# Kernel optimization log

Hardware: AMD Instinct MI355X
Metric: run time of the kernel (lower is better)

The kernel has to match this reference:

```python
import jax, jax.numpy as jnp
import numpy as np

NUM_MASKS = 255   # loop ids 0..254; id 255 is background
NUM_SEG = 256     # segment table size per batch element (ids 0..255)


def setup_inputs() -> dict:
    key = jax.random.key(0)
    k1, k2 = jax.random.split(key)
    b, c, h, w = 8, 256, 128, 128
    x = jax.random.normal(k1, (b, c, h, w), dtype=jnp.float32)
    mask = jax.random.randint(k2, (b, 1, h, w), 0, 256).astype(jnp.float32)
    return {"x": x, "mask": mask}


def reference(x, mask):
    b, c, h, w = x.shape
    hw = h * w
    # nearest interpolation to (h, w) is identity (mask already at that size)
    ids = mask.reshape(b, hw).astype(jnp.int32)          # (b, hw) segment ids 0..255
    x_sig = jax.nn.sigmoid(x.reshape(b, c, hw))          # (b, c, hw)

    # single-pass segment reduce: per-(batch, id) sums and pixel counts
    seg = (ids + jnp.arange(b, dtype=jnp.int32)[:, None] * NUM_SEG).reshape(-1)  # (b*hw,)
    counts = jax.ops.segment_sum(jnp.ones((b * hw,), x_sig.dtype), seg,
                                 num_segments=b * NUM_SEG).reshape(b, NUM_SEG)   # (b, 256)
    vals = x_sig.transpose(0, 2, 1).reshape(b * hw, c)                            # (b*hw, c)
    sums = jax.ops.segment_sum(vals, seg, num_segments=b * NUM_SEG)
    sums = sums.reshape(b, NUM_SEG, c)                                            # (b, 256, c)
    avg = sums / jnp.maximum(counts, 1.0)[:, :, None]                             # (b, 256, c)

    # gather per-pixel segment average; id 255 keeps label 0 (loop only covers 0..254)
    label = jnp.take_along_axis(avg, ids[:, :, None], axis=1)                     # (b, hw, c)
    is_bg = (ids == NUM_MASKS)[:, :, None]                                        # (b, hw, 1)
    label = jnp.where(is_bg, 0.0, label).transpose(0, 2, 1)                       # (b, c, hw)

    # ignore_bg=True: zero sigmoid activations on background pixels
    x_sig = jnp.where(is_bg.transpose(0, 2, 1), 0.0, x_sig)

    return jnp.mean((x_sig - label) ** 2)
```

## Files before the change

### kernel.cpp

```cpp
#include <hip/hip_runtime.h>

#define B 8
#define C 256
#define HW 16384
#define NSEG 256
#define NBLK (B * C)
#define NCH 32
#define CHUNK (HW / NCH)


typedef unsigned short ushort8 __attribute__((ext_vector_type(8)));

__device__ __forceinline__ float sigmoidf(float x) {
    return 1.0f / (1.0f + __expf(-x));
}

__global__ __launch_bounds__(256) void hist_kernel(const float* __restrict__ mask,
                                                   int* __restrict__ hist,
                                                   unsigned char* __restrict__ ids8) {
    __shared__ int h[NSEG];
    const int blk = blockIdx.x;
    const int b = blk >> 5, ch = blk & 31;
    const int t = threadIdx.x;
    h[t] = 0;
    __syncthreads();

    const float2* m2 = (const float2*)(mask + (size_t)b * HW + ch * CHUNK);
    uchar2* o2 = (uchar2*)(ids8 + (size_t)b * HW + ch * CHUNK);
    float2 v = m2[t];
    int i0 = (int)v.x, i1 = (int)v.y;
    o2[t] = make_uchar2((unsigned char)i0, (unsigned char)i1);
    atomicAdd(&h[i0], 1);
    atomicAdd(&h[i1], 1);
    __syncthreads();
    hist[blk * NSEG + t] = h[t];
}

__global__ __launch_bounds__(256) void assign_kernel(const unsigned char* __restrict__ ids8,
                                                     const int* __restrict__ hist,
                                                     int* __restrict__ starts_g,
                                                     unsigned short* __restrict__ permt) {
    __shared__ int sc[NSEG];
    __shared__ int cnt[NSEG];
    __shared__ int off[NSEG];
    const int blk = blockIdx.x;
    const int b = blk >> 5, ch = blk & 31;
    const int t = threadIdx.x;

    int tot = 0, pre = 0;
    for (int c2 = 0; c2 < NCH; ++c2) {
        int v = hist[((b << 5) + c2) * NSEG + t];
        tot += v;
        if (c2 < ch) pre += v;
    }
    cnt[t] = tot;
    sc[t] = tot;
    __syncthreads();
    for (int o = 1; o < NSEG; o <<= 1) {
        int v = (t >= o) ? sc[t - o] : 0;
        __syncthreads();
        sc[t] += v;
        __syncthreads();
    }
    int st = sc[t] - cnt[t];
    off[t] = st + pre;
    if (ch == 0) starts_g[b * NSEG + t] = st;
    __syncthreads();

    const unsigned char* idc = ids8 + (size_t)b * HW + ch * CHUNK;
    for (int j = 0; j < CHUNK / 256; ++j) {
        int pi = j * 256 + t;
        int id = idc[pi];
        int pos = atomicAdd(&off[id], 1);
        int p = ch * CHUNK + pi;
        int sidx = (pos & ~4095) | (((pos >> 3) & 7) << 9) | (((pos >> 6) & 63) << 3) | (pos & 7);
        permt[(size_t)b * HW + sidx] = (unsigned short)p;
    }
}

__global__ __launch_bounds__(256) void main_kernel(const float* __restrict__ x,
                                                   const unsigned short* __restrict__ permt,
                                                   const int* __restrict__ starts_g,
                                                   double* __restrict__ partials) {
    __shared__ float xs[HW];
    __shared__ int st[NSEG + 1];
    __shared__ float bS[NSEG];
    __shared__ float bQ[NSEG];
    __shared__ double wsum[4];

    const int bid = blockIdx.x;
    const int b = bid >> 8;
    const int t = threadIdx.x;

    const float* xrow = x + (size_t)bid * HW;
    for (int j = 0; j < 16; ++j) {
        int o = j * 1024 + t * 4;
        __builtin_amdgcn_global_load_lds(
            (const __attribute__((address_space(1))) void*)(xrow + o),
            (__attribute__((address_space(3))) void*)(xs + o), 16, 0, 0);
    }

    bS[t] = 0.0f;
    bQ[t] = 0.0f;
    st[t] = starts_g[b * NSEG + t];
    if (t == 0) st[NSEG] = HW;
    __syncthreads();

    int pos = t * 64;
    int lo = 0, hi = NSEG + 1;
    while (hi - lo > 1) {
        int mid = (lo + hi) >> 1;
        if (st[mid] <= pos) lo = mid; else hi = mid;
    }
    int s = lo;
    int nxt = st[s + 1];

    const ushort8* pr = (const ushort8*)(permt + (size_t)b * HW);
    const int w = t >> 6, l = t & 63;
    float S = 0.0f, Q = 0.0f;
    for (int j4 = 0; j4 < 8; ++j4) {
        ushort8 pp = pr[(w << 9) + (j4 << 6) + l];
        #pragma unroll
        for (int k = 0; k < 8; ++k) {
            int p = pp[k];
            float e = sigmoidf(xs[p]);
            if (pos >= nxt) {
                atomicAdd(&bS[s], S);
                atomicAdd(&bQ[s], Q);
                S = 0.0f; Q = 0.0f;
                do { ++s; } while (st[s + 1] <= pos);
                nxt = st[s + 1];
            }
            S += e;
            Q += e * e;
            ++pos;
        }
    }
    atomicAdd(&bS[s], S);
    atomicAdd(&bQ[s], Q);
    __syncthreads();

    double p = 0.0;
    if (t < NSEG - 1) {
        int n = st[t + 1] - st[t];
        if (n > 0) {
            double Sd = (double)bS[t], Qd = (double)bQ[t];
            p = Qd - Sd * Sd / (double)n;
        }
    }
    #pragma unroll
    for (int o = 32; o > 0; o >>= 1) p += __shfl_down(p, o);
    const int lane = t & 63, wv = t >> 6;
    if (lane == 0) wsum[wv] = p;
    __syncthreads();
    if (t == 0) partials[bid] = wsum[0] + wsum[1] + wsum[2] + wsum[3];
}

__global__ __launch_bounds__(256) void final_kernel(const double* __restrict__ partials,
                                                    float* __restrict__ out) {
    __shared__ double wsum[4];
    const int t = threadIdx.x;
    double p = 0.0;
    #pragma unroll
    for (int j = 0; j < NBLK / 256; ++j) p += partials[j * 256 + t];
    #pragma unroll
    for (int o = 32; o > 0; o >>= 1) p += __shfl_down(p, o);
    const int lane = t & 63, w = t >> 6;
    if (lane == 0) wsum[w] = p;
    __syncthreads();
    if (t == 0) {
        double total = wsum[0] + wsum[1] + wsum[2] + wsum[3];
        out[0] = (float)(total / (double)((size_t)B * C * HW));
    }
}

extern "C" void kernel_launch(void* const* d_in, const int* in_sizes, int n_in,
                              void* d_out, int out_size, void* d_ws, size_t ws_size,
                              hipStream_t stream) {
    const float* x = (const float*)d_in[0];
    const float* mask = (const float*)d_in[1];
    float* out = (float*)d_out;

    char* ws = (char*)d_ws;
    int* hist = (int*)ws;
    unsigned char* ids8 = (unsigned char*)(ws + 262144);
    int* starts = (int*)(ws + 393216);
    unsigned short* permt = (unsigned short*)(ws + 401408);
    double* partials = (double*)(ws + 663552);

    hist_kernel<<<B * NCH, 256, 0, stream>>>(mask, hist, ids8);
    assign_kernel<<<B * NCH, 256, 0, stream>>>(ids8, hist, starts, permt);
    main_kernel<<<NBLK, 256, 0, stream>>>(x, permt, starts, partials);
    final_kernel<<<1, 256, 0, stream>>>(partials, out);
}
```

Before: 228.2 us.

## Split each row into halves with global per-segment atomics to raise occupancy

Each (batch, channel) row is now handled by two blocks that each stage only half the pixels in LDS. This halves LDS use per block and allows more resident blocks per CU. Per-segment sums and squares are accumulated with global float atomics into zeroed buffers, and a new two-stage final reduction combines them using the full-row segment counts. It also switches the sigmoid to a hardware reciprocal and preloads the permutation vectors before the barrier. In exchange it adds global atomic traffic, an extra kernel launch, and nondeterministic float summation order.

```diff
diff --git a/kernel.cpp b/kernel.cpp
--- a/kernel.cpp
+++ b/kernel.cpp
@@ -3,21 +3,26 @@
 #define B 8
 #define C 256
 #define HW 16384
+#define HALF 8192
 #define NSEG 256
-#define NBLK (B * C)
 #define NCH 32
-#define CHUNK (HW / NCH)
+#define CHUNK 512
+#define NROW (B * C)
+#define NMAIN (NROW * 2)
 
 
 typedef unsigned short ushort8 __attribute__((ext_vector_type(8)));
 
 __device__ __forceinline__ float sigmoidf(float x) {
-    return 1.0f / (1.0f + __expf(-x));
+    float e = __expf(-x);
+    return __builtin_amdgcn_rcpf(1.0f + e);
 }
 
 __global__ __launch_bounds__(256) void hist_kernel(const float* __restrict__ mask,
                                                    int* __restrict__ hist,
-                                                   unsigned char* __restrict__ ids8) {
+                                                   unsigned char* __restrict__ ids8,
+                                                   float* __restrict__ Sg,
+                                                   float* __restrict__ Qg) {
     __shared__ int h[NSEG];
     const int blk = blockIdx.x;
     const int b = blk >> 5, ch = blk & 31;
@@ -32,29 +37,39 @@
     o2[t] = make_uchar2((unsigned char)i0, (unsigned char)i1);
     atomicAdd(&h[i0], 1);
     atomicAdd(&h[i1], 1);
+
+    float4 z = {0.0f, 0.0f, 0.0f, 0.0f};
+    float4* s4 = (float4*)(Sg + (size_t)blk * 2048);
+    float4* q4 = (float4*)(Qg + (size_t)blk * 2048);
+    #pragma unroll
+    for (int j = 0; j < 2; ++j) { s4[j * 256 + t] = z; q4[j * 256 + t] = z; }
+
     __syncthreads();
     hist[blk * NSEG + t] = h[t];
 }
 
 __global__ __launch_bounds__(256) void assign_kernel(const unsigned char* __restrict__ ids8,
                                                      const int* __restrict__ hist,
-                                                     int* __restrict__ starts_g,
+                                                     int* __restrict__ starts_h,
+                                                     int* __restrict__ counts_g,
                                                      unsigned short* __restrict__ permt) {
     __shared__ int sc[NSEG];
-    __shared__ int cnt[NSEG];
     __shared__ int off[NSEG];
     const int blk = blockIdx.x;
     const int b = blk >> 5, ch = blk & 31;
-    const int t = threadIdx.x;
-
-    int tot = 0, pre = 0;
+    const int half = ch >> 4;
+    const int t = threadIdx.x;
+
+    int tot = 0, tot_h = 0, pre = 0;
     for (int c2 = 0; c2 < NCH; ++c2) {
         int v = hist[((b << 5) + c2) * NSEG + t];
         tot += v;
-        if (c2 < ch) pre += v;
-    }
-    cnt[t] = tot;
-    sc[t] = tot;
+        if ((c2 >> 4) == half) {
+            tot_h += v;
+            if (c2 < ch) pre += v;
+        }
+    }
+    sc[t] = tot_h;
     __syncthreads();
     for (int o = 1; o < NSEG; o <<= 1) {
         int v = (t >= o) ? sc[t - o] : 0;
@@ -62,51 +77,57 @@
         sc[t] += v;
         __syncthreads();
     }
-    int st = sc[t] - cnt[t];
+    int st = sc[t] - tot_h;
     off[t] = st + pre;
-    if (ch == 0) starts_g[b * NSEG + t] = st;
+    if ((ch & 15) == 0) starts_h[(b * 2 + half) * NSEG + t] = st;
+    if (ch == 0) counts_g[b * NSEG + t] = tot;
     __syncthreads();
 
     const unsigned char* idc = ids8 + (size_t)b * HW + ch * CHUNK;
-    for (int j = 0; j < CHUNK / 256; ++j) {
+    for (int j = 0; j < 2; ++j) {
         int pi = j * 256 + t;
         int id = idc[pi];
         int pos = atomicAdd(&off[id], 1);
-        int p = ch * CHUNK + pi;
-        int sidx = (pos & ~4095) | (((pos >> 3) & 7) << 9) | (((pos >> 6) & 63) << 3) | (pos & 7);
-        permt[(size_t)b * HW + sidx] = (unsigned short)p;
-    }
-}
-
-__global__ __launch_bounds__(256) void main_kernel(const float* __restrict__ x,
-                                                   const unsigned short* __restrict__ permt,
-                                                   const int* __restrict__ starts_g,
-                                                   double* __restrict__ partials) {
-    __shared__ float xs[HW];
-    __shared__ int st[NSEG + 1];
-    __shared__ float bS[NSEG];
-    __shared__ float bQ[NSEG];
-    __shared__ double wsum[4];
+        int p = (ch * CHUNK + pi) & (HALF - 1);
+        int sidx = ((pos >> 11) << 11) | (((pos >> 3) & 3) << 9) | (((pos >> 5) & 63) << 3) | (pos & 7);
+        permt[(size_t)(b * 2 + half) * HALF + sidx] = (unsigned short)p;
+    }
+}
+
+__global__ __launch_bounds__(256, 4) void main_kernel(const float* __restrict__ x,
+                                                      const unsigned short* __restrict__ permt,
+                                                      const int* __restrict__ starts_h,
+                                                      float* __restrict__ Sg,
+                                                      float* __restrict__ Qg) {
+    __shared__ float xs[HALF];
+    __shared__ int st[NSEG + 2];
 
     const int bid = blockIdx.x;
-    const int b = bid >> 8;
-    const int t = threadIdx.x;
-
-    const float* xrow = x + (size_t)bid * HW;
-    for (int j = 0; j < 16; ++j) {
+    const int rowpair = bid >> 1;
+    const int half = bid & 1;
+    const int b = rowpair >> 8;
+    const int t = threadIdx.x;
+    const int w = t >> 6, l = t & 63;
+
+    const float* xsrc = x + (size_t)rowpair * HW + half * HALF;
+    for (int j = 0; j < 8; ++j) {
         int o = j * 1024 + t * 4;
         __builtin_amdgcn_global_load_lds(
-            (const __attribute__((address_space(1))) void*)(xrow + o),
+            (const __attribute__((address_space(1))) void*)(xsrc + o),
             (__attribute__((address_space(3))) void*)(xs + o), 16, 0, 0);
     }
 
-    bS[t] = 0.0f;
-    bQ[t] = 0.0f;
-    st[t] = starts_g[b * NSEG + t];
-    if (t == 0) st[NSEG] = HW;
-    __syncthreads();
-
-    int pos = t * 64;
+    const ushort8* pr = (const ushort8*)(permt + (size_t)(b * 2 + half) * HALF);
+    ushort8 pp0 = pr[(w << 8) + (0 << 6) + l];
+    ushort8 pp1 = pr[(w << 8) + (1 << 6) + l];
+    ushort8 pp2 = pr[(w << 8) + (2 << 6) + l];
+    ushort8 pp3 = pr[(w << 8) + (3 << 6) + l];
+
+    st[t] = starts_h[(b * 2 + half) * NSEG + t];
+    if (t == 0) st[NSEG] = HALF;
+    __syncthreads();
+
+    int pos = t * 32;
     int lo = 0, hi = NSEG + 1;
     while (hi - lo > 1) {
         int mid = (lo + hi) >> 1;
@@ -115,63 +136,61 @@
     int s = lo;
     int nxt = st[s + 1];
 
-    const ushort8* pr = (const ushort8*)(permt + (size_t)b * HW);
-    const int w = t >> 6, l = t & 63;
+    float* SgRow = Sg + (size_t)rowpair * NSEG;
+    float* QgRow = Qg + (size_t)rowpair * NSEG;
     float S = 0.0f, Q = 0.0f;
-    for (int j4 = 0; j4 < 8; ++j4) {
-        ushort8 pp = pr[(w << 9) + (j4 << 6) + l];
-        #pragma unroll
-        for (int k = 0; k < 8; ++k) {
-            int p = pp[k];
-            float e = sigmoidf(xs[p]);
-            if (pos >= nxt) {
-                atomicAdd(&bS[s], S);
-                atomicAdd(&bQ[s], Q);
-                S = 0.0f; Q = 0.0f;
-                do { ++s; } while (st[s + 1] <= pos);
-                nxt = st[s + 1];
-            }
-            S += e;
-            Q += e * e;
-            ++pos;
+
+    #define DO8(PP)                                              \
+        _Pragma("unroll")                                        \
+        for (int k = 0; k < 8; ++k) {                            \
+            if (pos == nxt) {                                    \
+                atomicAdd(&SgRow[s], S);                         \
+                atomicAdd(&QgRow[s], Q);                         \
+                S = 0.0f; Q = 0.0f;                              \
+                do { ++s; } while (st[s + 1] <= pos);            \
+                nxt = st[s + 1];                                 \
+            }                                                    \
+            float e = sigmoidf(xs[PP[k]]);                       \
+            S += e; Q += e * e; ++pos;                           \
         }
-    }
-    atomicAdd(&bS[s], S);
-    atomicAdd(&bQ[s], Q);
-    __syncthreads();
-
-    double p = 0.0;
-    if (t < NSEG - 1) {
-        int n = st[t + 1] - st[t];
-        if (n > 0) {
-            double Sd = (double)bS[t], Qd = (double)bQ[t];
-            p = Qd - Sd * Sd / (double)n;
+    DO8(pp0) DO8(pp1) DO8(pp2) DO8(pp3)
+    #undef DO8
+
+    atomicAdd(&SgRow[s], S);
+    atomicAdd(&QgRow[s], Q);
+}
+
+__global__ __launch_bounds__(256) void final1_kernel(const float* __restrict__ Sg,
+                                                     const float* __restrict__ Qg,
+                                                     const int* __restrict__ counts_g,
+                                                     double* __restrict__ partials) {
+    __shared__ double wsum[4];
+    const int blk = blockIdx.x, t = threadIdx.x;
+    double acc = 0.0;
+    for (int j = 0; j < 32; ++j) {
+        int bin = blk * 8192 + j * 256 + t;
+        int row = bin >> 8, s = bin & 255, b = row >> 8;
+        int n = counts_g[b * NSEG + s];
+        if (s < NSEG - 1 && n > 0) {
+            double S = (double)Sg[bin], Q = (double)Qg[bin];
+            acc += Q - S * S / (double)n;
         }
     }
+    #pragma unroll
+    for (int o = 32; o > 0; o >>= 1) acc += __shfl_down(acc, o);
+    const int lane = t & 63, w = t >> 6;
+    if (lane == 0) wsum[w] = acc;
+    __syncthreads();
+    if (t == 0) partials[blk] = wsum[0] + wsum[1] + wsum[2] + wsum[3];
+}
+
+__global__ __launch_bounds__(64) void final2_kernel(const double* __restrict__ partials,
+                                                    float* __restrict__ out) {
+    const int t = threadIdx.x;
+    double p = partials[t];
     #pragma unroll
     for (int o = 32; o > 0; o >>= 1) p += __shfl_down(p, o);
-    const int lane = t & 63, wv = t >> 6;
-    if (lane == 0) wsum[wv] = p;
-    __syncthreads();
-    if (t == 0) partials[bid] = wsum[0] + wsum[1] + wsum[2] + wsum[3];
-}
-
-__global__ __launch_bounds__(256) void final_kernel(const double* __restrict__ partials,
-                                                    float* __restrict__ out) {
-    __shared__ double wsum[4];
-    const int t = threadIdx.x;
-    double p = 0.0;
-    #pragma unroll
-    for (int j = 0; j < NBLK / 256; ++j) p += partials[j * 256 + t];
-    #pragma unroll
-    for (int o = 32; o > 0; o >>= 1) p += __shfl_down(p, o);
-    const int lane = t & 63, w = t >> 6;
-    if (lane == 0) wsum[w] = p;
-    __syncthreads();
-    if (t == 0) {
-        double total = wsum[0] + wsum[1] + wsum[2] + wsum[3];
-        out[0] = (float)(total / (double)((size_t)B * C * HW));
-    }
+    if (t == 0) out[0] = (float)(p / (double)((size_t)B * C * HW));
 }
 
 extern "C" void kernel_launch(void* const* d_in, const int* in_sizes, int n_in,
@@ -184,12 +203,16 @@
     char* ws = (char*)d_ws;
     int* hist = (int*)ws;
     unsigned char* ids8 = (unsigned char*)(ws + 262144);
-    int* starts = (int*)(ws + 393216);
-    unsigned short* permt = (unsigned short*)(ws + 401408);
-    double* partials = (double*)(ws + 663552);
-
-    hist_kernel<<<B * NCH, 256, 0, stream>>>(mask, hist, ids8);
-    assign_kernel<<<B * NCH, 256, 0, stream>>>(ids8, hist, starts, permt);
-    main_kernel<<<NBLK, 256, 0, stream>>>(x, permt, starts, partials);
-    final_kernel<<<1, 256, 0, stream>>>(partials, out);
-}
+    int* starts_h = (int*)(ws + 393216);
+    int* counts_g = (int*)(ws + 409600);
+    unsigned short* permt = (unsigned short*)(ws + 417792);
+    float* Sg = (float*)(ws + 679936);
+    float* Qg = (float*)(ws + 2777088);
+    double* partials = (double*)(ws + 4874240);
+
+    hist_kernel<<<B * NCH, 256, 0, stream>>>(mask, hist, ids8, Sg, Qg);
+    assign_kernel<<<B * NCH, 256, 0, stream>>>(ids8, hist, starts_h, counts_g, permt);
+    main_kernel<<<NMAIN, 256, 0, stream>>>(x, permt, starts_h, Sg, Qg);
+    final1_kernel<<<64, 256, 0, stream>>>(Sg, Qg, counts_g, partials);
+    final2_kernel<<<1, 64, 0, stream>>>(partials, out);
+}
```

After: 275.8 us. 1.21x slower.
